# Performance work log

Measured on AMD Instinct MI355X. Metric: run time of the kernel, lower is better.

## Reference

```python
import jax, jax.numpy as jnp
import numpy as np

BS, P, M, K, C, H = 128, 16, 64, 4, 21, 256  # batch, papers, matrix_size, kernel, bins(out_ch), hidden
HO = (M - K) // K + 1  # 16 output positions per dim (stride == kernel)
L = HO * HO            # 256 patches
KK = K * K             # 16 elems per patch (in_channels=1)
FLAT = HO * P * C      # 5376 = linear_flatten in-dim
SIGMA = 0.1


def _mus():
    # histogram bin centers from KernelConv2d.__init__
    bin_size = 2.0 / (C - 1)
    mus = [1.0, 1.0 - bin_size / 2]
    for i in range(1, C - 1):
        mus.append(mus[i] - bin_size)
    return jnp.asarray(mus, jnp.float32)  # [C]


def setup_inputs() -> dict:
    key = jax.random.key(0)
    ks = jax.random.split(key, 16)
    def lin(k, fan_in, fan_out):
        kw, kb = jax.random.split(k)
        bound = 1.0 / np.sqrt(fan_in)
        W = jax.random.uniform(kw, (fan_in, fan_out), jnp.float32, -bound, bound)
        b = jax.random.uniform(kb, (fan_out,), jnp.float32, -bound, bound)
        return W, b
    W_flat, b_flat = lin(ks[0], FLAT, H)
    W_attn, b_attn = lin(ks[1], H, 1)
    W_fadd, b_fadd = lin(ks[2], 17, H)
    W_d1, b_d1 = lin(ks[3], H, H)
    W_d2, b_d2 = lin(ks[4], H, 2)
    return {
        "sim_mat": jax.random.uniform(ks[5], (BS, P, M, M), jnp.float32),
        "f_add": jax.random.normal(ks[6], (BS, 17), jnp.float32),
        "W_flat": W_flat, "b_flat": b_flat,
        "W_attn": W_attn, "b_attn": b_attn,
        "W_fadd": W_fadd, "b_fadd": b_fadd,
        "W_d1": W_d1, "b_d1": b_d1,
        "W_d2": W_d2, "b_d2": b_d2,
        "weight_feature": jnp.zeros((1,), jnp.float32),
    }


def reference(sim_mat, f_add, W_flat, b_flat, W_attn, b_attn, W_fadd, b_fadd,
              W_d1, b_d1, W_d2, b_d2, weight_feature):
    mus = _mus()
    bs = sim_mat.shape[0]
    # im2col: stride == kernel, no padding -> plain block reshape. Patch order (ho, wo) row-major matches F.unfold.
    patches = sim_mat.reshape(bs, P, HO, K, HO, K)
    patches = jnp.transpose(patches, (0, 1, 2, 4, 3, 5)).reshape(bs, P, L, KK)
    # Gaussian RBF soft histogram: conv weight is mus[oc] broadcast over the patch, sigma=0.1 everywhere.
    diff = patches[..., None] - mus                      # [bs,P,L,KK,C]
    rbf = jnp.exp(-(diff * diff) / (2.0 * SIGMA * SIGMA)).sum(axis=3)  # [bs,P,L,C]
    g = 0.01 * jnp.log(jnp.clip(rbf, 1e-10))
    g = jnp.tanh(g).reshape(bs, P, HO, HO, C)            # (b,P,ho,wo,C)
    # torch: stack -> (b,P,C,ho,wo); transpose(1,3) -> (b,ho,C,P,wo); reshape(b,ho,-1)
    x = jnp.transpose(g, (0, 2, 4, 1, 3)).reshape(bs, HO, FLAT)
    h1 = jnp.tanh(x @ W_flat + b_flat)                   # [bs,HO,H]
    attn = jax.nn.softmax(h1 @ W_attn + b_attn, axis=1)  # [bs,HO,1]
    logits_coarse = jnp.tanh((attn * h1).sum(axis=1))    # [bs,H]
    f_add_proj = jnp.tanh(f_add @ W_fadd + b_fadd)       # [bs,H]
    s = jax.nn.sigmoid(weight_feature[0])
    combined = (1.0 - s) * f_add_proj + s * logits_coarse  # esb, aminer branch
    score = jnp.tanh(combined @ W_d1 + b_d1)
    out = score @ W_d2 + b_d2                            # [bs,2]
    return (jax.nn.log_softmax(out, axis=1), out)
```

## Files before the change

kernel.cpp:

```cpp
#include <hip/hip_runtime.h>
#include <hip/hip_bf16.h>
#include <math.h>

#define BSZ   128
#define NP    16
#define NC    21
#define NH    256
#define HOUT  16
#define NFLAT 5376

#define XT_STRIDE 680
#define XT_BYTES  (32 * XT_STRIDE * 2)
#define PSTR      (2048 * 256)

typedef __attribute__((ext_vector_type(4))) float f32x4;
typedef __attribute__((ext_vector_type(8))) short bf16x8;

__device__ __forceinline__ ushort f2bf(float v) {
    __hip_bfloat16 h = __float2bfloat16(v);
    return *reinterpret_cast<ushort*>(&h);
}

__device__ __forceinline__ float hist_act(float s) {
    float u = 0.01f * __logf(fmaxf(s, 1e-10f));
    float u2 = u * u;
    return u * (1.f + u2 * (-0.33333333f + 0.13333333f * u2));
}

__device__ __forceinline__ float fast_tanh(float v) {
    float e = __expf(2.f * v);
    return 1.f - 2.f * __builtin_amdgcn_rcpf(e + 1.f);
}

__global__ __launch_bounds__(256) void k_prep(const float* __restrict__ W,
                                              ushort* __restrict__ WtF) {
    int id = blockIdx.x * 256 + threadIdx.x;
    int l = id & 63;
    int ks = id >> 10;
    int n = (((id >> 6) & 15) << 4) + (l & 15);
    int kb = ks * 32 + (l >> 4) * 8;
    ushort v[8];
#pragma unroll
    for (int e = 0; e < 8; ++e) {
        int kp = kb + e;
        int p = kp / 336;
        int rem = kp - p * 336;
        int c = rem >> 4, wo = rem & 15;
        int ksrc = c * 256 + p * 16 + wo;
        v[e] = f2bf(W[(size_t)ksrc * NH + n]);
    }
    *(uint4*)(WtF + (size_t)id * 8) = *(uint4*)v;
}

extern "C" __global__ __launch_bounds__(1024, 8) void k_fused(
    const float* __restrict__ sim,
    const ushort* __restrict__ WtF,
    float* __restrict__ part)
{
    extern __shared__ __align__(16) char smem[];
    ushort* xT = (ushort*)smem;
    const int bid = blockIdx.x;
    const int bm = bid >> 3, sk = bid & 7;
    const int tid = threadIdx.x;

    {
        int w = tid >> 6, l = tid & 63;
        int tile = w >> 2, q = w & 3;
        int boff = tile >> 1, poff = tile & 1;
        int wo = l & 15, ho = q * 4 + (l >> 4);

        const float* src = sim
            + (((size_t)(2 * bm + boff)) * 16 + (2 * sk + poff)) * 4096
            + (size_t)(ho * 4) * 64 + wo * 4;
        float4 ebuf[4];
#pragma unroll
        for (int i = 0; i < 4; ++i) ebuf[i] = *(const float4*)(src + i * 64);

        float f[16], g[16];
        float s0[4];
#pragma unroll
        for (int i = 0; i < 4; ++i) {
            float4 e4 = ebuf[i];
            float pa = 0.f, pb = 0.f;
#pragma unroll
            for (int jj = 0; jj < 4; ++jj) {
                float e = (jj == 0) ? e4.x : (jj == 1) ? e4.y : (jj == 2) ? e4.z : e4.w;
                int k2 = i * 4 + jj;
                float d0 = e - 1.0f;
                float t0 = __expf(-50.f * d0 * d0);
                if (jj & 1) pb += t0; else pa += t0;
                float d1 = e - 0.95f;
                f[k2] = __expf(-50.f * d1 * d1);
                g[k2] = __expf(-10.f * d1 - 0.5f);
            }
            s0[i] = pa + pb;
        }
        float sum0 = (s0[0] + s0[1]) + (s0[2] + s0[3]);
        ushort* xrow = xT + (boff * 16 + ho) * XT_STRIDE + poff * 336 + wo;
        xrow[0] = f2bf(hist_act(sum0));

#pragma unroll
        for (int c = 1; c < 21; ++c) {
            float t01 = f[0] + f[1],  t23 = f[2] + f[3];
            float t45 = f[4] + f[5],  t67 = f[6] + f[7];
            float t89 = f[8] + f[9],  tab = f[10] + f[11];
            float tcd = f[12] + f[13], tef = f[14] + f[15];
            float u0 = t01 + t23, u1 = t45 + t67;
            float u2 = t89 + tab, u3 = tcd + tef;
            float sv = (u0 + u1) + (u2 + u3);
            xrow[c * 16] = f2bf(hist_act(sv));
            if (c < 20) {
#pragma unroll
                for (int k2 = 0; k2 < 16; ++k2) { f[k2] *= g[k2]; g[k2] *= 0.36787944117f; }
            }
        }
    }
    __syncthreads();

    {
        int l = tid & 63, w = tid >> 6;
        int wr = w >> 3, wc = w & 7;
        int lr = l & 15, lk = l >> 4;
        int arow = wr * 16 + lr;
        const char* aBase = (const char*)xT + arow * (XT_STRIDE * 2);

        const ushort* gB = WtF + (((size_t)(sk * 21) * 16 + wc * 2) * 64 + l) * 8;

        f32x4 acc[2];
        acc[0] = (f32x4){0.f, 0.f, 0.f, 0.f};
        acc[1] = (f32x4){0.f, 0.f, 0.f, 0.f};

#pragma unroll
        for (int kt = 0; kt < 21; ++kt) {
            bf16x8 a = *(const bf16x8*)(aBase + kt * 64 + lk * 16);
#pragma unroll
            for (int nt = 0; nt < 2; ++nt) {
                bf16x8 bb = *(const bf16x8*)(gB + ((size_t)kt * 16 + nt) * 512);
                acc[nt] = __builtin_amdgcn_mfma_f32_16x16x32_bf16(a, bb, acc[nt], 0, 0, 0);
            }
        }

        float* pp = part + (size_t)sk * PSTR;
        int crow = bm * 32 + wr * 16 + lk * 4;
#pragma unroll
        for (int nt = 0; nt < 2; ++nt) {
            int ccol = wc * 32 + nt * 16 + lr;
#pragma unroll
            for (int j = 0; j < 4; ++j)
                pp[(size_t)(crow + j) * 256 + ccol] = acc[nt][j];
        }
    }
}

__global__ __launch_bounds__(512) void k_head(
    const float* __restrict__ part,
    const float* __restrict__ b_flat,
    const float* __restrict__ f_add,
    const float* __restrict__ W_attn,
    const float* __restrict__ b_attn,
    const float* __restrict__ W_fadd,
    const float* __restrict__ b_fadd,
    const float* __restrict__ W_d1,
    const float* __restrict__ b_d1,
    const float* __restrict__ W_d2,
    const float* __restrict__ b_d2,
    const float* __restrict__ wfeat,
    float* __restrict__ out)
{
    const int b = blockIdx.x;
    const int tid = threadIdx.x;

    __shared__ float sh1[16 * 256];
    __shared__ float slog[16];
    __shared__ float scomb[256];
    __shared__ float scpart[512];
    __shared__ float r01[8];

#pragma unroll
    for (int i = 0; i < 8; ++i) {
        int idx = i * 512 + tid;
        int row = idx >> 8, col = idx & 255;
        size_t prow = (size_t)(b * 16 + row) * 256 + col;
        float v = b_flat[col];
#pragma unroll
        for (int s = 0; s < 8; ++s) v += part[(size_t)s * PSTR + prow];
        sh1[idx] = fast_tanh(v);
    }
    __syncthreads();

    if (tid < 256) {
        int ho = tid >> 4, j = tid & 15;
        float sv = 0.f;
#pragma unroll
        for (int t2 = 0; t2 < 16; ++t2)
            sv += sh1[ho * 256 + j + t2 * 16] * W_attn[j + t2 * 16];
        sv += __shfl_xor(sv, 1); sv += __shfl_xor(sv, 2);
        sv += __shfl_xor(sv, 4); sv += __shfl_xor(sv, 8);
        if (j == 0) slog[ho] = sv + b_attn[0];
    }
    __syncthreads();

    if (tid < 256) {
        float attnv[16];
        float mx = -1e30f;
#pragma unroll
        for (int t2 = 0; t2 < 16; ++t2) mx = fmaxf(mx, slog[t2]);
        float sum = 0.f;
#pragma unroll
        for (int t2 = 0; t2 < 16; ++t2) { attnv[t2] = __expf(slog[t2] - mx); sum += attnv[t2]; }
        float inv = __builtin_amdgcn_rcpf(sum);

        float lc = 0.f;
#pragma unroll
        for (int t2 = 0; t2 < 16; ++t2) lc += attnv[t2] * inv * sh1[t2 * 256 + tid];
        lc = fast_tanh(lc);

        float fp = b_fadd[tid];
#pragma unroll
        for (int k = 0; k < 17; ++k) fp += f_add[b * 17 + k] * W_fadd[k * 256 + tid];
        fp = fast_tanh(fp);

        float sg = __builtin_amdgcn_rcpf(1.f + __expf(-wfeat[0]));
        scomb[tid] = (1.f - sg) * fp + sg * lc;
    }
    __syncthreads();

    {
        int n = tid & 255, half = tid >> 8;
        float sc = 0.f;
        int k0 = half * 128;
#pragma unroll 8
        for (int k = 0; k < 128; ++k) sc += scomb[k0 + k] * W_d1[(k0 + k) * 256 + n];
        scpart[half * 256 + n] = sc;
    }
    __syncthreads();

    if (tid < 256) {
        float sc = fast_tanh(scpart[tid] + scpart[256 + tid] + b_d1[tid]);
        float p0 = sc * W_d2[tid * 2 + 0];
        float p1 = sc * W_d2[tid * 2 + 1];
#pragma unroll
        for (int off = 1; off < 64; off <<= 1) {
            p0 += __shfl_xor(p0, off);
            p1 += __shfl_xor(p1, off);
        }
        if ((tid & 63) == 0) { r01[tid >> 6] = p0; r01[4 + (tid >> 6)] = p1; }
    }
    __syncthreads();

    if (tid == 0) {
        float o0 = r01[0] + r01[1] + r01[2] + r01[3] + b_d2[0];
        float o1 = r01[4] + r01[5] + r01[6] + r01[7] + b_d2[1];
        float mx = fmaxf(o0, o1);
        float lse = mx + __logf(__expf(o0 - mx) + __expf(o1 - mx));
        out[b * 2 + 0] = o0 - lse;
        out[b * 2 + 1] = o1 - lse;
        out[256 + b * 2 + 0] = o0;
        out[256 + b * 2 + 1] = o1;
    }
}

extern "C" void kernel_launch(void* const* d_in, const int* in_sizes, int n_in,
                              void* d_out, int out_size, void* d_ws, size_t ws_size,
                              hipStream_t stream) {
    const float* sim    = (const float*)d_in[0];
    const float* f_add  = (const float*)d_in[1];
    const float* W_flat = (const float*)d_in[2];
    const float* b_flat = (const float*)d_in[3];
    const float* W_attn = (const float*)d_in[4];
    const float* b_attn = (const float*)d_in[5];
    const float* W_fadd = (const float*)d_in[6];
    const float* b_fadd = (const float*)d_in[7];
    const float* W_d1   = (const float*)d_in[8];
    const float* b_d1   = (const float*)d_in[9];
    const float* W_d2   = (const float*)d_in[10];
    const float* b_d2   = (const float*)d_in[11];
    const float* wfeat  = (const float*)d_in[12];
    float* out = (float*)d_out;

    ushort* WtF = (ushort*)d_ws;
    float* part = (float*)(WtF + (size_t)256 * NFLAT);

    hipLaunchKernelGGL(k_prep, dim3(672), dim3(256), 0, stream, W_flat, WtF);
    hipLaunchKernelGGL(k_fused, dim3(512), dim3(1024), XT_BYTES, stream, sim, WtF, part);
    hipLaunchKernelGGL(k_head, dim3(128), dim3(512), 0, stream,
                       part, b_flat, f_add, W_attn, b_attn, W_fadd, b_fadd,
                       W_d1, b_d1, W_d2, b_d2, wfeat, out);
}
```

Before: 51.39 us.

## Fuse head into main kernel via last-block atomic counter; share B loads across rows

```diff
diff --git a/kernel.cpp b/kernel.cpp
--- a/kernel.cpp
+++ b/kernel.cpp
@@ -52,108 +52,10 @@
     *(uint4*)(WtF + (size_t)id * 8) = *(uint4*)v;
 }
 
-extern "C" __global__ __launch_bounds__(1024, 8) void k_fused(
+extern "C" __global__ __launch_bounds__(1024, 8) void k_all(
     const float* __restrict__ sim,
     const ushort* __restrict__ WtF,
-    float* __restrict__ part)
-{
-    extern __shared__ __align__(16) char smem[];
-    ushort* xT = (ushort*)smem;
-    const int bid = blockIdx.x;
-    const int bm = bid >> 3, sk = bid & 7;
-    const int tid = threadIdx.x;
-
-    {
-        int w = tid >> 6, l = tid & 63;
-        int tile = w >> 2, q = w & 3;
-        int boff = tile >> 1, poff = tile & 1;
-        int wo = l & 15, ho = q * 4 + (l >> 4);
-
-        const float* src = sim
-            + (((size_t)(2 * bm + boff)) * 16 + (2 * sk + poff)) * 4096
-            + (size_t)(ho * 4) * 64 + wo * 4;
-        float4 ebuf[4];
-#pragma unroll
-        for (int i = 0; i < 4; ++i) ebuf[i] = *(const float4*)(src + i * 64);
-
-        float f[16], g[16];
-        float s0[4];
-#pragma unroll
-        for (int i = 0; i < 4; ++i) {
-            float4 e4 = ebuf[i];
-            float pa = 0.f, pb = 0.f;
-#pragma unroll
-            for (int jj = 0; jj < 4; ++jj) {
-                float e = (jj == 0) ? e4.x : (jj == 1) ? e4.y : (jj == 2) ? e4.z : e4.w;
-                int k2 = i * 4 + jj;
-                float d0 = e - 1.0f;
-                float t0 = __expf(-50.f * d0 * d0);
-                if (jj & 1) pb += t0; else pa += t0;
-                float d1 = e - 0.95f;
-                f[k2] = __expf(-50.f * d1 * d1);
-                g[k2] = __expf(-10.f * d1 - 0.5f);
-            }
-            s0[i] = pa + pb;
-        }
-        float sum0 = (s0[0] + s0[1]) + (s0[2] + s0[3]);
-        ushort* xrow = xT + (boff * 16 + ho) * XT_STRIDE + poff * 336 + wo;
-        xrow[0] = f2bf(hist_act(sum0));
-
-#pragma unroll
-        for (int c = 1; c < 21; ++c) {
-            float t01 = f[0] + f[1],  t23 = f[2] + f[3];
-            float t45 = f[4] + f[5],  t67 = f[6] + f[7];
-            float t89 = f[8] + f[9],  tab = f[10] + f[11];
-            float tcd = f[12] + f[13], tef = f[14] + f[15];
-            float u0 = t01 + t23, u1 = t45 + t67;
-            float u2 = t89 + tab, u3 = tcd + tef;
-            float sv = (u0 + u1) + (u2 + u3);
-            xrow[c * 16] = f2bf(hist_act(sv));
-            if (c < 20) {
-#pragma unroll
-                for (int k2 = 0; k2 < 16; ++k2) { f[k2] *= g[k2]; g[k2] *= 0.36787944117f; }
-            }
-        }
-    }
-    __syncthreads();
-
-    {
-        int l = tid & 63, w = tid >> 6;
-        int wr = w >> 3, wc = w & 7;
-        int lr = l & 15, lk = l >> 4;
-        int arow = wr * 16 + lr;
-        const char* aBase = (const char*)xT + arow * (XT_STRIDE * 2);
-
-        const ushort* gB = WtF + (((size_t)(sk * 21) * 16 + wc * 2) * 64 + l) * 8;
-
-        f32x4 acc[2];
-        acc[0] = (f32x4){0.f, 0.f, 0.f, 0.f};
-        acc[1] = (f32x4){0.f, 0.f, 0.f, 0.f};
-
-#pragma unroll
-        for (int kt = 0; kt < 21; ++kt) {
-            bf16x8 a = *(const bf16x8*)(aBase + kt * 64 + lk * 16);
-#pragma unroll
-            for (int nt = 0; nt < 2; ++nt) {
-                bf16x8 bb = *(const bf16x8*)(gB + ((size_t)kt * 16 + nt) * 512);
-                acc[nt] = __builtin_amdgcn_mfma_f32_16x16x32_bf16(a, bb, acc[nt], 0, 0, 0);
-            }
-        }
-
-        float* pp = part + (size_t)sk * PSTR;
-        int crow = bm * 32 + wr * 16 + lk * 4;
-#pragma unroll
-        for (int nt = 0; nt < 2; ++nt) {
-            int ccol = wc * 32 + nt * 16 + lr;
-#pragma unroll
-            for (int j = 0; j < 4; ++j)
-                pp[(size_t)(crow + j) * 256 + ccol] = acc[nt][j];
-        }
-    }
-}
-
-__global__ __launch_bounds__(512) void k_head(
-    const float* __restrict__ part,
+    float* __restrict__ part,
     const float* __restrict__ b_flat,
     const float* __restrict__ f_add,
     const float* __restrict__ W_attn,
@@ -165,98 +67,199 @@
     const float* __restrict__ W_d2,
     const float* __restrict__ b_d2,
     const float* __restrict__ wfeat,
-    float* __restrict__ out)
+    float* __restrict__ out,
+    uint* __restrict__ cnt)
 {
-    const int b = blockIdx.x;
+    extern __shared__ __align__(16) char smem[];
+    ushort* xT = (ushort*)smem;
+    __shared__ uint lastFlag;
+    const int bid = blockIdx.x;
+    const int bm = bid >> 3, sk = bid & 7;
     const int tid = threadIdx.x;
 
-    __shared__ float sh1[16 * 256];
-    __shared__ float slog[16];
-    __shared__ float scomb[256];
-    __shared__ float scpart[512];
-    __shared__ float r01[8];
-
-#pragma unroll
-    for (int i = 0; i < 8; ++i) {
-        int idx = i * 512 + tid;
-        int row = idx >> 8, col = idx & 255;
-        size_t prow = (size_t)(b * 16 + row) * 256 + col;
-        float v = b_flat[col];
-#pragma unroll
-        for (int s = 0; s < 8; ++s) v += part[(size_t)s * PSTR + prow];
-        sh1[idx] = fast_tanh(v);
+    {
+        int w = tid >> 6, l = tid & 63;
+        int tile = w >> 2, q = w & 3;
+        int boff = tile >> 1, poff = tile & 1;
+        int wo = l & 15, ho = q * 4 + (l >> 4);
+
+        const float* src = sim
+            + (((size_t)(2 * bm + boff)) * 16 + (2 * sk + poff)) * 4096
+            + (size_t)(ho * 4) * 64 + wo * 4;
+        float4 ebuf[4];
+#pragma unroll
+        for (int i = 0; i < 4; ++i) ebuf[i] = *(const float4*)(src + i * 64);
+
+        float f[16], g[16];
+        float s0[4];
+#pragma unroll
+        for (int i = 0; i < 4; ++i) {
+            float4 e4 = ebuf[i];
+            float pa = 0.f, pb = 0.f;
+#pragma unroll
+            for (int jj = 0; jj < 4; ++jj) {
+                float e = (jj == 0) ? e4.x : (jj == 1) ? e4.y : (jj == 2) ? e4.z : e4.w;
+                int k2 = i * 4 + jj;
+                float d0 = e - 1.0f;
+                float t0 = __expf(-50.f * d0 * d0);
+                if (jj & 1) pb += t0; else pa += t0;
+                float d1 = e - 0.95f;
+                f[k2] = __expf(-50.f * d1 * d1);
+                g[k2] = __expf(-10.f * d1 - 0.5f);
+            }
+            s0[i] = pa + pb;
+        }
+        float sum0 = (s0[0] + s0[1]) + (s0[2] + s0[3]);
+        ushort* xrow = xT + (boff * 16 + ho) * XT_STRIDE + poff * 336 + wo;
+        xrow[0] = f2bf(hist_act(sum0));
+
+#pragma unroll
+        for (int c = 1; c < 21; ++c) {
+            float t01 = f[0] + f[1],  t23 = f[2] + f[3];
+            float t45 = f[4] + f[5],  t67 = f[6] + f[7];
+            float t89 = f[8] + f[9],  tab = f[10] + f[11];
+            float tcd = f[12] + f[13], tef = f[14] + f[15];
+            float u0 = t01 + t23, u1 = t45 + t67;
+            float u2 = t89 + tab, u3 = tcd + tef;
+            float sv = (u0 + u1) + (u2 + u3);
+            xrow[c * 16] = f2bf(hist_act(sv));
+            if (c < 20) {
+#pragma unroll
+                for (int k2 = 0; k2 < 16; ++k2) { f[k2] *= g[k2]; g[k2] *= 0.36787944117f; }
+            }
+        }
     }
     __syncthreads();
 
-    if (tid < 256) {
-        int ho = tid >> 4, j = tid & 15;
-        float sv = 0.f;
-#pragma unroll
-        for (int t2 = 0; t2 < 16; ++t2)
-            sv += sh1[ho * 256 + j + t2 * 16] * W_attn[j + t2 * 16];
-        sv += __shfl_xor(sv, 1); sv += __shfl_xor(sv, 2);
-        sv += __shfl_xor(sv, 4); sv += __shfl_xor(sv, 8);
-        if (j == 0) slog[ho] = sv + b_attn[0];
-    }
+    {
+        int l = tid & 63, w = tid >> 6;
+        int lr = l & 15, lk = l >> 4;
+        const char* aBase0 = (const char*)xT + lr * (XT_STRIDE * 2);
+        const char* aBase1 = (const char*)xT + (16 + lr) * (XT_STRIDE * 2);
+
+        const ushort* gB = WtF + (((size_t)(sk * 21) * 16 + w) * 64 + l) * 8;
+
+        f32x4 acc0 = (f32x4){0.f, 0.f, 0.f, 0.f};
+        f32x4 acc1 = (f32x4){0.f, 0.f, 0.f, 0.f};
+
+#pragma unroll
+        for (int kt = 0; kt < 21; ++kt) {
+            bf16x8 bb = *(const bf16x8*)(gB + (size_t)kt * 8192);
+            bf16x8 a0 = *(const bf16x8*)(aBase0 + kt * 64 + lk * 16);
+            bf16x8 a1 = *(const bf16x8*)(aBase1 + kt * 64 + lk * 16);
+            acc0 = __builtin_amdgcn_mfma_f32_16x16x32_bf16(a0, bb, acc0, 0, 0, 0);
+            acc1 = __builtin_amdgcn_mfma_f32_16x16x32_bf16(a1, bb, acc1, 0, 0, 0);
+        }
+
+        float* pp = part + (size_t)sk * PSTR;
+        int ccol = w * 16 + lr;
+        int crow0 = bm * 32 + lk * 4;
+#pragma unroll
+        for (int j = 0; j < 4; ++j) {
+            pp[(size_t)(crow0 + j) * 256 + ccol] = acc0[j];
+            pp[(size_t)(crow0 + 16 + j) * 256 + ccol] = acc1[j];
+        }
+    }
+
     __syncthreads();
-
-    if (tid < 256) {
-        float attnv[16];
-        float mx = -1e30f;
-#pragma unroll
-        for (int t2 = 0; t2 < 16; ++t2) mx = fmaxf(mx, slog[t2]);
-        float sum = 0.f;
-#pragma unroll
-        for (int t2 = 0; t2 < 16; ++t2) { attnv[t2] = __expf(slog[t2] - mx); sum += attnv[t2]; }
-        float inv = __builtin_amdgcn_rcpf(sum);
-
-        float lc = 0.f;
-#pragma unroll
-        for (int t2 = 0; t2 < 16; ++t2) lc += attnv[t2] * inv * sh1[t2 * 256 + tid];
-        lc = fast_tanh(lc);
-
-        float fp = b_fadd[tid];
-#pragma unroll
-        for (int k = 0; k < 17; ++k) fp += f_add[b * 17 + k] * W_fadd[k * 256 + tid];
-        fp = fast_tanh(fp);
-
-        float sg = __builtin_amdgcn_rcpf(1.f + __expf(-wfeat[0]));
-        scomb[tid] = (1.f - sg) * fp + sg * lc;
+    if (tid == 0) {
+        uint old = __hip_atomic_fetch_add(&cnt[bm], 1u, __ATOMIC_ACQ_REL,
+                                          __HIP_MEMORY_SCOPE_AGENT);
+        lastFlag = (old == 7u) ? 1u : 0u;
     }
     __syncthreads();
+    if (!lastFlag) return;
 
     {
-        int n = tid & 255, half = tid >> 8;
-        float sc = 0.f;
-        int k0 = half * 128;
+        int g = tid >> 9, t = tid & 511;
+        int b = 2 * bm + g;
+        float* base = (float*)smem + g * 4896;
+        float* sh1    = base;
+        float* slog   = base + 4096;
+        float* scomb  = base + 4112;
+        float* scpart = base + 4368;
+        float* r01    = base + 4880;
+
+#pragma unroll
+        for (int i = 0; i < 8; ++i) {
+            int idx = i * 512 + t;
+            int row = idx >> 8, col = idx & 255;
+            size_t prow = (size_t)(b * 16 + row) * 256 + col;
+            float v = b_flat[col];
+#pragma unroll
+            for (int s = 0; s < 8; ++s) v += part[(size_t)s * PSTR + prow];
+            sh1[idx] = fast_tanh(v);
+        }
+        __syncthreads();
+
+        if (t < 256) {
+            int ho = t >> 4, j = t & 15;
+            float sv = 0.f;
+#pragma unroll
+            for (int t2 = 0; t2 < 16; ++t2)
+                sv += sh1[ho * 256 + j + t2 * 16] * W_attn[j + t2 * 16];
+            sv += __shfl_xor(sv, 1); sv += __shfl_xor(sv, 2);
+            sv += __shfl_xor(sv, 4); sv += __shfl_xor(sv, 8);
+            if (j == 0) slog[ho] = sv + b_attn[0];
+        }
+        __syncthreads();
+
+        if (t < 256) {
+            float mx = -1e30f;
+#pragma unroll
+            for (int t2 = 0; t2 < 16; ++t2) mx = fmaxf(mx, slog[t2]);
+            float sum = 0.f, lc = 0.f;
+#pragma unroll
+            for (int t2 = 0; t2 < 16; ++t2) {
+                float e = __expf(slog[t2] - mx);
+                sum += e;
+                lc += e * sh1[t2 * 256 + t];
+            }
+            lc = fast_tanh(lc * __builtin_amdgcn_rcpf(sum));
+
+            float fp = b_fadd[t];
+#pragma unroll
+            for (int k = 0; k < 17; ++k) fp += f_add[b * 17 + k] * W_fadd[k * 256 + t];
+            fp = fast_tanh(fp);
+
+            float sg = __builtin_amdgcn_rcpf(1.f + __expf(-wfeat[0]));
+            scomb[t] = (1.f - sg) * fp + sg * lc;
+        }
+        __syncthreads();
+
+        {
+            int n = t & 255, half = t >> 8;
+            float sc = 0.f;
+            int k0 = half * 128;
 #pragma unroll 8
-        for (int k = 0; k < 128; ++k) sc += scomb[k0 + k] * W_d1[(k0 + k) * 256 + n];
-        scpart[half * 256 + n] = sc;
-    }
-    __syncthreads();
-
-    if (tid < 256) {
-        float sc = fast_tanh(scpart[tid] + scpart[256 + tid] + b_d1[tid]);
-        float p0 = sc * W_d2[tid * 2 + 0];
-        float p1 = sc * W_d2[tid * 2 + 1];
-#pragma unroll
-        for (int off = 1; off < 64; off <<= 1) {
-            p0 += __shfl_xor(p0, off);
-            p1 += __shfl_xor(p1, off);
-        }
-        if ((tid & 63) == 0) { r01[tid >> 6] = p0; r01[4 + (tid >> 6)] = p1; }
-    }
-    __syncthreads();
-
-    if (tid == 0) {
-        float o0 = r01[0] + r01[1] + r01[2] + r01[3] + b_d2[0];
-        float o1 = r01[4] + r01[5] + r01[6] + r01[7] + b_d2[1];
-        float mx = fmaxf(o0, o1);
-        float lse = mx + __logf(__expf(o0 - mx) + __expf(o1 - mx));
-        out[b * 2 + 0] = o0 - lse;
-        out[b * 2 + 1] = o1 - lse;
-        out[256 + b * 2 + 0] = o0;
-        out[256 + b * 2 + 1] = o1;
+            for (int k = 0; k < 128; ++k) sc += scomb[k0 + k] * W_d1[(k0 + k) * 256 + n];
+            scpart[half * 256 + n] = sc;
+        }
+        __syncthreads();
+
+        if (t < 256) {
+            float sc = fast_tanh(scpart[t] + scpart[256 + t] + b_d1[t]);
+            float p0 = sc * W_d2[t * 2 + 0];
+            float p1 = sc * W_d2[t * 2 + 1];
+#pragma unroll
+            for (int off = 1; off < 64; off <<= 1) {
+                p0 += __shfl_xor(p0, off);
+                p1 += __shfl_xor(p1, off);
+            }
+            if ((t & 63) == 0) { r01[t >> 6] = p0; r01[4 + (t >> 6)] = p1; }
+        }
+        __syncthreads();
+
+        if (t == 0) {
+            float o0 = r01[0] + r01[1] + r01[2] + r01[3] + b_d2[0];
+            float o1 = r01[4] + r01[5] + r01[6] + r01[7] + b_d2[1];
+            float mx = fmaxf(o0, o1);
+            float lse = mx + __logf(__expf(o0 - mx) + __expf(o1 - mx));
+            out[b * 2 + 0] = o0 - lse;
+            out[b * 2 + 1] = o1 - lse;
+            out[256 + b * 2 + 0] = o0;
+            out[256 + b * 2 + 1] = o1;
+        }
     }
 }
 
@@ -280,10 +283,12 @@
 
     ushort* WtF = (ushort*)d_ws;
     float* part = (float*)(WtF + (size_t)256 * NFLAT);
-
+    uint* cnt = (uint*)((char*)d_ws + (36u << 20));
+
+    hipMemsetAsync(cnt, 0, 64 * sizeof(uint), stream);
     hipLaunchKernelGGL(k_prep, dim3(672), dim3(256), 0, stream, W_flat, WtF);
-    hipLaunchKernelGGL(k_fused, dim3(512), dim3(1024), XT_BYTES, stream, sim, WtF, part);
-    hipLaunchKernelGGL(k_head, dim3(128), dim3(512), 0, stream,
-                       part, b_flat, f_add, W_attn, b_attn, W_fadd, b_fadd,
-                       W_d1, b_d1, W_d2, b_d2, wfeat, out);
-}
+    hipLaunchKernelGGL(k_all, dim3(512), dim3(1024), XT_BYTES, stream,
+                       sim, WtF, part,
+                       b_flat, f_add, W_attn, b_attn, W_fadd, b_fadd,
+                       W_d1, b_d1, W_d2, b_d2, wfeat, out, cnt);
+}
```

Result: slower. 76.72 us (+49.3%).
